# Optimization experiments

Measured on AMD Instinct MI355X. Metric: run time of the kernel, lower is better.

The kernel has to match this reference:

```python
import jax, jax.numpy as jnp
import numpy as np

N = 65536      # nodes
E = 32768      # edges
H = 256        # hidden_features
B = 64         # graphs
NPG = 1024     # nodes per graph
K = 24         # padded subgraph index width
ELEM = 24      # 2 * len(ORDERED_ELEMENT_LIST_WITH_HYDROGEN) (assumed 12 elements)
EMB = 200
STAT = 32
D = 2 * H + (2 * H + ELEM) + EMB + STAT  # 1280, dense hidden dim
OUT = 512
DEPTH = 3


def setup_inputs() -> dict:
    key = jax.random.key(0)
    ks = jax.random.split(key, 12)
    X = jax.random.normal(ks[0], (N, H), jnp.float32)
    edge_index = jax.random.randint(ks[1], (2, E), 0, N)
    batch_vec = jnp.arange(N) // NPG                  # node -> graph id (sorted)
    ptr = jnp.arange(B + 1) * NPG                     # graph node offsets
    subgraph_idx_left = jax.random.randint(ks[2], (E, K), -1, NPG)   # -1 = padding
    subgraph_idx_right = jax.random.randint(ks[3], (E, K), -1, NPG)
    edge_elem_comp = jax.random.uniform(ks[4], (E, ELEM), jnp.float32)
    edge_embedding = jax.random.normal(ks[5], (E, EMB), jnp.float32)
    static_edge_features = jax.random.normal(ks[6], (E, STAT), jnp.float32)
    s = 1.0 / np.sqrt(D)
    Wd = jax.random.normal(ks[7], (DEPTH, D, D), jnp.float32) * s
    bd = jax.random.normal(ks[8], (DEPTH, D), jnp.float32) * s
    Wo = jax.random.normal(ks[9], (D, OUT), jnp.float32) * s
    bo = jax.random.normal(ks[10], (OUT,), jnp.float32) * s
    return dict(X=X, edge_index=edge_index, batch_vec=batch_vec, ptr=ptr,
                subgraph_idx_left=subgraph_idx_left, subgraph_idx_right=subgraph_idx_right,
                edge_elem_comp=edge_elem_comp, edge_embedding=edge_embedding,
                static_edge_features=static_edge_features, Wd=Wd, bd=bd, Wo=Wo, bo=bo)


def _mean_pool(X, idx_abs, num_edges):
    # masked segment-mean of node rows into per-edge slots (global_mean_pool)
    e, k = idx_abs.shape
    seg = jnp.repeat(jnp.arange(e), k)                # edge id per flattened index
    flat = idx_abs.reshape(-1)
    mask = (flat != -1).astype(X.dtype)               # mask after ptr offset, as in source
    gathered = X[flat] * mask[:, None]                # negative idx wraps, matching torch
    sums = jax.ops.segment_sum(gathered, seg, num_segments=num_edges)
    counts = jax.ops.segment_sum(mask, seg, num_segments=num_edges)
    return jnp.where(counts[:, None] > 0, sums / jnp.maximum(counts, 1.0)[:, None], 0.0)


def reference(X, edge_index, batch_vec, ptr, subgraph_idx_left, subgraph_idx_right,
              edge_elem_comp, edge_embedding, static_edge_features, Wd, bd, Wo, bo):
    src, dst = edge_index[0], edge_index[1]
    node_pairs = jnp.concatenate([X[src], X[dst]], axis=1)            # [E, 2H]
    edge_batch_map = batch_vec[src]                                   # [E]
    off = ptr[edge_batch_map][:, None]                                # [E, 1]
    pooled_left = _mean_pool(X, subgraph_idx_left + off, E)           # [E, H]
    pooled_right = _mean_pool(X, subgraph_idx_right + off, E)         # [E, H]
    feats = jnp.concatenate([node_pairs, pooled_left, pooled_right, edge_elem_comp,
                             edge_embedding, static_edge_features], axis=1)  # [E, D]
    h = feats
    for i in range(Wd.shape[0]):
        h = jax.nn.elu(h @ Wd[i] + bd[i]) + h         # ELU + residual (dropout=0 eval)
    return h @ Wo + bo
```

## Files before the change

### kernel.cpp

```cpp
#include <hip/hip_runtime.h>
#include <math.h>

#define NN   65536
#define EE   32768
#define HH   256
#define KK   24
#define DDIM 1280
#define OUTD 512
#define KT   (DDIM / 32)
#define GCAP 1024

typedef _Float16 half8 __attribute__((ext_vector_type(8)));
typedef _Float16 half4 __attribute__((ext_vector_type(4)));
typedef float    f32x4 __attribute__((ext_vector_type(4)));

__device__ __forceinline__ float elu1(float x) { return x > 0.f ? x : expm1f(x); }

__device__ __forceinline__ void gl16(const void* g, void* l) {
    __builtin_amdgcn_global_load_lds(
        (const __attribute__((address_space(1))) void*)g,
        (__attribute__((address_space(3))) void*)l, 16, 0, 0);
}

__global__ __launch_bounds__(256) void prep_kernel(
    const float* __restrict__ Wd, const float* __restrict__ Wo,
    const float* __restrict__ X,
    _Float16* __restrict__ W16d, _Float16* __restrict__ W16o,
    _Float16* __restrict__ X16, int* __restrict__ cnt)
{
    const int b = blockIdx.x;
    const int lane = threadIdx.x & 63;
    if (b < 2400) {
        const int l = b / 800;
        const int s = (b % 800) * 4 + (threadIdx.x >> 6);
        const int nt = s & 7, nb = (s >> 3) % 10, kt = s / 80;
        const int kbase = kt * 32 + 8 * (lane >> 4);
        const int n     = nb * 128 + nt * 16 + (lane & 15);
        const float* W = Wd + (size_t)l * DDIM * DDIM;
        half8 v;
        #pragma unroll
        for (int j = 0; j < 8; ++j) v[j] = (_Float16)W[(size_t)(kbase + j) * DDIM + n];
        ((half8*)(W16d + (size_t)l * DDIM * DDIM))[(size_t)s * 64 + lane] = v;
    } else if (b < 2720) {
        const int s = (b - 2400) * 4 + (threadIdx.x >> 6);
        const int nt = s & 7, nb = (s >> 3) % 4, kt = s / 32;
        const int kbase = kt * 32 + 8 * (lane >> 4);
        const int n     = nb * 128 + nt * 16 + (lane & 15);
        half8 v;
        #pragma unroll
        for (int j = 0; j < 8; ++j) v[j] = (_Float16)Wo[(size_t)(kbase + j) * OUTD + n];
        ((half8*)W16o)[(size_t)s * 64 + lane] = v;
    } else if (b == 2720) {
        if (threadIdx.x < 64) cnt[threadIdx.x] = 0;
    } else {
        const int a = b - 2721;
        const int r  = a * 16 + (threadIdx.x >> 4);
        const int c0 = (threadIdx.x & 15) * 16;
        const float4* s4 = (const float4*)(X + (size_t)r * HH + c0);
        const float4 f0 = s4[0], f1 = s4[1], f2 = s4[2], f3 = s4[3];
        half8 o0, o1;
        o0[0]=(_Float16)f0.x; o0[1]=(_Float16)f0.y; o0[2]=(_Float16)f0.z; o0[3]=(_Float16)f0.w;
        o0[4]=(_Float16)f1.x; o0[5]=(_Float16)f1.y; o0[6]=(_Float16)f1.z; o0[7]=(_Float16)f1.w;
        o1[0]=(_Float16)f2.x; o1[1]=(_Float16)f2.y; o1[2]=(_Float16)f2.z; o1[3]=(_Float16)f2.w;
        o1[4]=(_Float16)f3.x; o1[5]=(_Float16)f3.y; o1[6]=(_Float16)f3.z; o1[7]=(_Float16)f3.w;
        *(half8*)(X16 + (size_t)r * HH + c0)     = o0;
        *(half8*)(X16 + (size_t)r * HH + c0 + 8) = o1;
    }
}

__global__ __launch_bounds__(256) void scatter_kernel(
    const int* __restrict__ src_idx, const int* __restrict__ batch_vec,
    int* __restrict__ perm, int* __restrict__ cnt, int nE)
{
    __shared__ int lc[64];
    __shared__ int lbase[64];
    const int tid = threadIdx.x;
    if (tid < 64) lc[tid] = 0;
    __syncthreads();
    const int e = blockIdx.x * 256 + tid;
    int g = -1, li = 0;
    if (e < nE) {
        g = batch_vec[src_idx[e]];
        li = atomicAdd(&lc[g], 1);
    }
    __syncthreads();
    if (tid < 64 && lc[tid] > 0) lbase[tid] = atomicAdd(&cnt[tid], lc[tid]);
    __syncthreads();
    if (e >= nE) return;
    const int idx = lbase[g] + li;
    if (idx < GCAP) perm[g * GCAP + idx] = e;
}

__global__ __launch_bounds__(256) void feats16_kernel(
    const _Float16* __restrict__ X16, const int* __restrict__ perm,
    const int* __restrict__ cnt,
    const int* __restrict__ src_idx, const int* __restrict__ dst_idx,
    const int* __restrict__ ptrv,
    const int* __restrict__ sl, const int* __restrict__ sr,
    const float* __restrict__ elem, const float* __restrict__ emb,
    const float* __restrict__ stat,
    _Float16* __restrict__ F16)
{
    const int b  = blockIdx.x;
    const int x  = b & 7;
    const int j  = b >> 3;
    const int g  = x + 8 * (j >> 8);
    const int jj = j & 255;
    const int slot = jj * 4 + (threadIdx.x >> 6);
    const int ng = min(cnt[g], GCAP);
    if (slot >= ng) return;
    const int e = perm[g * GCAP + slot];

    const int lane = threadIdx.x & 63;
    const int src  = src_idx[e];
    const int dst  = dst_idx[e];
    const int off  = ptrv[g];

    const half4* Xh = (const half4*)X16;

    const size_t hb = ((size_t)(e >> 7) * 40) * 4096
                    + (size_t)((e & 127) >> 4) * 512
                    + (size_t)((e & 15) + (((lane >> 1) & 3) << 4)) * 8 + (lane & 1) * 4;
    const size_t hkt = (size_t)(lane >> 3) * 4096;
#define STH(seg, hv)                                                          \
    *(half4*)(F16 + hb + ((size_t)(seg) * 8) * 4096 + hkt) = (hv);
#define STF(seg, v)                                                           \
    {                                                                         \
        half4 h_;                                                             \
        h_[0] = (_Float16)(v).x; h_[1] = (_Float16)(v).y;                     \
        h_[2] = (_Float16)(v).z; h_[3] = (_Float16)(v).w;                     \
        STH(seg, h_);                                                         \
    }

    STH(0, Xh[(size_t)src * 64 + lane]);
    STH(1, Xh[(size_t)dst * 64 + lane]);

    float4 sL = make_float4(0.f, 0.f, 0.f, 0.f);
    float4 sR = make_float4(0.f, 0.f, 0.f, 0.f);
    int cL = 0, cR = 0;
    #pragma unroll
    for (int k = 0; k < KK; ++k) {
        const int il  = sl[e * KK + k] + off;
        const int ir  = sr[e * KK + k] + off;
        const int okL = il >= 0;
        const int okR = ir >= 0;
        const float wL = okL ? 1.f : 0.f;
        const float wR = okR ? 1.f : 0.f;
        const half4 vl = Xh[(size_t)(okL ? il : 0) * 64 + lane];
        const half4 vr = Xh[(size_t)(okR ? ir : 0) * 64 + lane];
        sL.x += (float)vl[0] * wL; sL.y += (float)vl[1] * wL;
        sL.z += (float)vl[2] * wL; sL.w += (float)vl[3] * wL;
        sR.x += (float)vr[0] * wR; sR.y += (float)vr[1] * wR;
        sR.z += (float)vr[2] * wR; sR.w += (float)vr[3] * wR;
        cL += okL; cR += okR;
    }
    const float rL = cL > 0 ? 1.f / (float)cL : 0.f;
    const float rR = cR > 0 ? 1.f / (float)cR : 0.f;
    STF(2, make_float4(sL.x * rL, sL.y * rL, sL.z * rL, sL.w * rL));
    STF(3, make_float4(sR.x * rR, sR.y * rR, sR.z * rR, sR.w * rR));

    float4 tail;
    if (lane < 6)       tail = ((const float4*)(elem + (size_t)e * 24))[lane];
    else if (lane < 56) tail = ((const float4*)(emb  + (size_t)e * 200))[lane - 6];
    else                tail = ((const float4*)(stat + (size_t)e * 32))[lane - 56];
    STF(4, tail);
#undef STF
#undef STH
}

template<bool RESID, bool OUT32, bool H16>
__global__ __launch_bounds__(256) void mfma_gemm7(
    const _Float16* __restrict__ A16,
    const _Float16* __restrict__ W16, const float* __restrict__ bias,
    float* __restrict__ C32, _Float16* __restrict__ C16,
    int N, int nbN)
{
    __shared__ __align__(16) char sA[3][8192];
    __shared__ __align__(16) char sB[3][8192];

    const int t    = threadIdx.x;
    const int wid  = t >> 6;
    const int lane = t & 63;

    int m_t, n_t;
    if ((gridDim.y & 7) == 0) {
        const int flat = blockIdx.y * gridDim.x + blockIdx.x;
        m_t = (flat & 7) + 8 * (flat / (8 * gridDim.x));
        n_t = (flat >> 3) % gridDim.x;
    } else {
        m_t = blockIdx.y; n_t = blockIdx.x;
    }

    f32x4 acc[2][8];
    #pragma unroll
    for (int i = 0; i < 2; ++i)
        #pragma unroll
        for (int j = 0; j < 8; ++j) acc[i][j] = (f32x4){0.f, 0.f, 0.f, 0.f};

    _Float16 resv[4][2][2][4];

    const char* Abase = (const char*)A16 + (size_t)m_t * KT * 8192;
    const char* Bbase = (const char*)W16;

#define STAGE(d, ktv)                                                           \
    {                                                                           \
        const char* Ak = Abase + (size_t)(ktv) * 8192 + wid * 1024 + lane * 16; \
        const char* Bk = Bbase + ((size_t)(ktv) * nbN + n_t) * 8192             \
                         + wid * 1024 + lane * 16;                              \
        gl16(Ak,        sA[d] + wid * 1024);                                    \
        gl16(Ak + 4096, sA[d] + (4 + wid) * 1024);                              \
        gl16(Bk,        sB[d] + wid * 1024);                                    \
        gl16(Bk + 4096, sB[d] + (4 + wid) * 1024);                              \
    }

    STAGE(0, 0);
    STAGE(1, 1);
    STAGE(2, 2);

    int cur = 0;
    for (int kt = 0; kt < KT; ++kt) {
        if (kt + 2 < KT)      asm volatile("s_waitcnt vmcnt(8)" ::: "memory");
        else if (kt + 1 < KT) asm volatile("s_waitcnt vmcnt(4)" ::: "memory");
        else                  asm volatile("s_waitcnt vmcnt(0)" ::: "memory");
        __builtin_amdgcn_sched_barrier(0);
        __builtin_amdgcn_s_barrier();
        __builtin_amdgcn_sched_barrier(0);

        const half8* pa = (const half8*)sA[cur];
        const half8* pb = (const half8*)sB[cur];
        const half8 af0 = pa[(2 * wid)     * 64 + lane];
        const half8 af1 = pa[(2 * wid + 1) * 64 + lane];
        half8 bf[8];
        #pragma unroll
        for (int j = 0; j < 8; ++j) bf[j] = pb[j * 64 + lane];

        if (RESID) {
            #pragma unroll
            for (int q = 0; q < 4; ++q) {
                if (kt == n_t * 4 + q) {
                    #pragma unroll
                    for (int i = 0; i < 2; ++i)
                        #pragma unroll
                        for (int jj = 0; jj < 2; ++jj)
                            #pragma unroll
                            for (int r = 0; r < 4; ++r) {
                                const int chunk = ((lane >> 4) * 4 + r)
                                                + 16 * (jj * 2 + ((lane >> 3) & 1));
                                resv[q][i][jj][r] = *(const _Float16*)
                                    (sA[cur] + (wid * 2 + i) * 1024
                                             + chunk * 16 + (lane & 7) * 2);
                            }
                }
            }
        }

        asm volatile("s_waitcnt lgkmcnt(0)" ::: "memory");
        __builtin_amdgcn_sched_barrier(0);
        __builtin_amdgcn_s_barrier();
        __builtin_amdgcn_sched_barrier(0);

        if (kt + 3 < KT) STAGE(cur, kt + 3);
        __builtin_amdgcn_sched_barrier(0);

        __builtin_amdgcn_s_setprio(1);
        #pragma unroll
        for (int j = 0; j < 8; ++j) {
            acc[0][j] = __builtin_amdgcn_mfma_f32_16x16x32_f16(af0, bf[j], acc[0][j], 0, 0, 0);
            acc[1][j] = __builtin_amdgcn_mfma_f32_16x16x32_f16(af1, bf[j], acc[1][j], 0, 0, 0);
        }
        __builtin_amdgcn_s_setprio(0);

        cur = (cur == 2) ? 0 : cur + 1;
    }
#undef STAGE

    if (H16) {
        char* Cb = (char*)C16 + ((size_t)m_t * 40 + n_t * 4) * 8192;
        #pragma unroll
        for (int q = 0; q < 4; ++q) {
            #pragma unroll
            for (int i = 0; i < 2; ++i)
                #pragma unroll
                for (int jj = 0; jj < 2; ++jj) {
                    const int j = 2 * q + jj;
                    const int col = n_t * 128 + j * 16 + (lane & 15);
                    const float bv = bias[col];
                    #pragma unroll
                    for (int r = 0; r < 4; ++r) {
                        float v = acc[i][j][r] + bv;
                        v = elu1(v) + (float)resv[q][i][jj][r];
                        const int chunk = ((lane >> 4) * 4 + r)
                                        + 16 * (jj * 2 + ((lane >> 3) & 1));
                        *(_Float16*)(sA[0] + (wid * 2 + i) * 1024
                                           + chunk * 16 + (lane & 7) * 2)
                            = (_Float16)v;
                    }
                }
            __syncthreads();
            *(uint4*)(Cb + (size_t)q * 8192 + t * 32) =
                *(const uint4*)(sA[0] + t * 32);
            *(uint4*)(Cb + (size_t)q * 8192 + t * 32 + 16) =
                *(const uint4*)(sA[0] + t * 32 + 16);
            __syncthreads();
        }
    } else {
        const int m0 = m_t * 128;
        #pragma unroll
        for (int i = 0; i < 2; ++i) {
            #pragma unroll
            for (int j = 0; j < 8; ++j) {
                const int col = n_t * 128 + j * 16 + (lane & 15);
                const float bv = bias[col];
                #pragma unroll
                for (int r = 0; r < 4; ++r) {
                    const int row = m0 + wid * 32 + i * 16 + (lane >> 4) * 4 + r;
                    float v = acc[i][j][r] + bv;
                    if (OUT32) C32[(size_t)row * N + col] = v;
                }
            }
        }
    }
}

extern "C" void kernel_launch(void* const* d_in, const int* in_sizes, int n_in,
                              void* d_out, int out_size, void* d_ws, size_t ws_size,
                              hipStream_t stream) {
    const float* X          = (const float*)d_in[0];
    const int*   edge_index = (const int*)d_in[1];
    const int*   batch_vec  = (const int*)d_in[2];
    const int*   ptrv       = (const int*)d_in[3];
    const int*   sl         = (const int*)d_in[4];
    const int*   sr         = (const int*)d_in[5];
    const float* elem       = (const float*)d_in[6];
    const float* emb        = (const float*)d_in[7];
    const float* stat       = (const float*)d_in[8];
    const float* Wd         = (const float*)d_in[9];
    const float* bd         = (const float*)d_in[10];
    const float* Wo         = (const float*)d_in[11];
    const float* bo         = (const float*)d_in[12];
    float* out = (float*)d_out;

    _Float16* W16d = (_Float16*)d_ws;
    _Float16* W16o = W16d + (size_t)3 * DDIM * DDIM;
    _Float16* X16  = W16o + (size_t)DDIM * OUTD;
    int* perm = (int*)(X16 + (size_t)NN * HH);
    int* cnt  = perm + (size_t)64 * GCAP;
    char* hbase = (char*)(cnt + 64);
    hbase = (char*)(((size_t)hbase + 255) & ~(size_t)255);
    const size_t rem = ws_size - (size_t)(hbase - (char*)d_ws);

    int CH = EE;
    while (CH > 2048 && (size_t)CH * DDIM * 4 > rem) CH >>= 1;
    _Float16* f16a = (_Float16*)hbase;
    _Float16* f16b = f16a + (size_t)CH * DDIM;

    prep_kernel<<<2721 + NN / 16, 256, 0, stream>>>(Wd, Wo, X, W16d, W16o, X16, cnt);

    for (int e0 = 0; e0 < EE; e0 += CH) {
        scatter_kernel<<<CH / 256, 256, 0, stream>>>(
            edge_index + e0, batch_vec, perm, cnt, CH);

        feats16_kernel<<<64 * (GCAP / 4), 256, 0, stream>>>(
            X16, perm, cnt, edge_index + e0, edge_index + EE + e0, ptrv,
            sl + (size_t)e0 * KK, sr + (size_t)e0 * KK,
            elem + (size_t)e0 * 24, emb + (size_t)e0 * 200,
            stat + (size_t)e0 * 32, f16a);

        dim3 gd(10, CH / 128);
        mfma_gemm7<true, false, true><<<gd, 256, 0, stream>>>(
            f16a, W16d + 0 * (size_t)DDIM * DDIM, bd + 0 * DDIM,
            nullptr, f16b, DDIM, 10);
        mfma_gemm7<true, false, true><<<gd, 256, 0, stream>>>(
            f16b, W16d + 1 * (size_t)DDIM * DDIM, bd + 1 * DDIM,
            nullptr, f16a, DDIM, 10);
        mfma_gemm7<true, false, true><<<gd, 256, 0, stream>>>(
            f16a, W16d + 2 * (size_t)DDIM * DDIM, bd + 2 * DDIM,
            nullptr, f16b, DDIM, 10);

        dim3 go(4, CH / 128);
        mfma_gemm7<false, true, false><<<go, 256, 0, stream>>>(
            f16b, W16o, bo, out + (size_t)e0 * OUTD, nullptr, OUTD, 4);
    }
}
```

Before: 704.8 us.

## Compact edges by graph, stage feature rows in LDS, unpermute on output

Adds prefix and compact kernels that build a dense graph-sorted edge ordering. The feature kernel processes 16 sorted edges per block, stages their rows in shared memory, and writes coalesced tiles into the GEMM's tiled A layout. Rows are no longer scattered by edge id. The final GEMM scatters output rows back to original edge order through the permutation. The aim is better locality for the node gathers and coalesced feature writes, at the cost of two extra small launches and scattered output stores. The sperm identity initialisation in prep appears to be overwritten by compact.

```diff
diff --git a/kernel.cpp b/kernel.cpp
--- a/kernel.cpp
+++ b/kernel.cpp
@@ -9,6 +9,7 @@
 #define OUTD 512
 #define KT   (DDIM / 32)
 #define GCAP 1024
+#define RSTRIDE 1296
 
 typedef _Float16 half8 __attribute__((ext_vector_type(8)));
 typedef _Float16 half4 __attribute__((ext_vector_type(4)));
@@ -26,7 +27,8 @@
     const float* __restrict__ Wd, const float* __restrict__ Wo,
     const float* __restrict__ X,
     _Float16* __restrict__ W16d, _Float16* __restrict__ W16o,
-    _Float16* __restrict__ X16, int* __restrict__ cnt)
+    _Float16* __restrict__ X16, int* __restrict__ cnt,
+    int* __restrict__ sperm)
 {
     const int b = blockIdx.x;
     const int lane = threadIdx.x & 63;
@@ -52,7 +54,7 @@
         ((half8*)W16o)[(size_t)s * 64 + lane] = v;
     } else if (b == 2720) {
         if (threadIdx.x < 64) cnt[threadIdx.x] = 0;
-    } else {
+    } else if (b < 6817) {
         const int a = b - 2721;
         const int r  = a * 16 + (threadIdx.x >> 4);
         const int c0 = (threadIdx.x & 15) * 16;
@@ -65,6 +67,10 @@
         o1[4]=(_Float16)f3.x; o1[5]=(_Float16)f3.y; o1[6]=(_Float16)f3.z; o1[7]=(_Float16)f3.w;
         *(half8*)(X16 + (size_t)r * HH + c0)     = o0;
         *(half8*)(X16 + (size_t)r * HH + c0 + 8) = o1;
+    } else {
+        const int i0 = (b - 6817) * 1024 + threadIdx.x * 4;
+        if (i0 < EE)
+            *(int4*)(sperm + i0) = make_int4(i0, i0 + 1, i0 + 2, i0 + 3);
     }
 }
 
@@ -91,81 +97,116 @@
     if (idx < GCAP) perm[g * GCAP + idx] = e;
 }
 
-__global__ __launch_bounds__(256) void feats16_kernel(
-    const _Float16* __restrict__ X16, const int* __restrict__ perm,
-    const int* __restrict__ cnt,
+__global__ __launch_bounds__(64) void prefix_kernel(
+    const int* __restrict__ cnt, int* __restrict__ prefixv)
+{
+    if (threadIdx.x == 0) {
+        int acc = 0;
+        for (int g = 0; g < 64; ++g) {
+            prefixv[g] = acc;
+            acc += min(cnt[g], GCAP);
+        }
+        prefixv[64] = acc;
+    }
+}
+
+__global__ __launch_bounds__(256) void compact_kernel(
+    const int* __restrict__ perm, const int* __restrict__ cnt,
+    const int* __restrict__ prefixv, int* __restrict__ sperm)
+{
+    const int id = blockIdx.x * 256 + threadIdx.x;
+    const int g = id >> 10, idx = id & (GCAP - 1);
+    if (idx < min(cnt[g], GCAP))
+        sperm[prefixv[g] + idx] = perm[id];
+}
+
+__global__ __launch_bounds__(256) void feats16t_kernel(
+    const _Float16* __restrict__ X16, const int* __restrict__ sperm,
     const int* __restrict__ src_idx, const int* __restrict__ dst_idx,
-    const int* __restrict__ ptrv,
+    const int* __restrict__ batch_vec, const int* __restrict__ ptrv,
     const int* __restrict__ sl, const int* __restrict__ sr,
     const float* __restrict__ elem, const float* __restrict__ emb,
     const float* __restrict__ stat,
     _Float16* __restrict__ F16)
 {
-    const int b  = blockIdx.x;
-    const int x  = b & 7;
-    const int j  = b >> 3;
-    const int g  = x + 8 * (j >> 8);
-    const int jj = j & 255;
-    const int slot = jj * 4 + (threadIdx.x >> 6);
-    const int ng = min(cnt[g], GCAP);
-    if (slot >= ng) return;
-    const int e = perm[g * GCAP + slot];
-
+    __shared__ _Float16 rows[16][RSTRIDE];
+
+    const int p  = blockIdx.x;
+    int lb = p;
+    if ((gridDim.x & 7) == 0) {
+        const int chunkb = gridDim.x >> 3;
+        lb = (p & 7) * chunkb + (p >> 3);
+    }
+    const int wv   = threadIdx.x >> 6;
     const int lane = threadIdx.x & 63;
-    const int src  = src_idx[e];
-    const int dst  = dst_idx[e];
-    const int off  = ptrv[g];
+    const int s0   = lb * 16;
 
     const half4* Xh = (const half4*)X16;
 
-    const size_t hb = ((size_t)(e >> 7) * 40) * 4096
-                    + (size_t)((e & 127) >> 4) * 512
-                    + (size_t)((e & 15) + (((lane >> 1) & 3) << 4)) * 8 + (lane & 1) * 4;
-    const size_t hkt = (size_t)(lane >> 3) * 4096;
-#define STH(seg, hv)                                                          \
-    *(half4*)(F16 + hb + ((size_t)(seg) * 8) * 4096 + hkt) = (hv);
-#define STF(seg, v)                                                           \
-    {                                                                         \
-        half4 h_;                                                             \
-        h_[0] = (_Float16)(v).x; h_[1] = (_Float16)(v).y;                     \
-        h_[2] = (_Float16)(v).z; h_[3] = (_Float16)(v).w;                     \
-        STH(seg, h_);                                                         \
-    }
-
-    STH(0, Xh[(size_t)src * 64 + lane]);
-    STH(1, Xh[(size_t)dst * 64 + lane]);
-
-    float4 sL = make_float4(0.f, 0.f, 0.f, 0.f);
-    float4 sR = make_float4(0.f, 0.f, 0.f, 0.f);
-    int cL = 0, cR = 0;
     #pragma unroll
-    for (int k = 0; k < KK; ++k) {
-        const int il  = sl[e * KK + k] + off;
-        const int ir  = sr[e * KK + k] + off;
-        const int okL = il >= 0;
-        const int okR = ir >= 0;
-        const float wL = okL ? 1.f : 0.f;
-        const float wR = okR ? 1.f : 0.f;
-        const half4 vl = Xh[(size_t)(okL ? il : 0) * 64 + lane];
-        const half4 vr = Xh[(size_t)(okR ? ir : 0) * 64 + lane];
-        sL.x += (float)vl[0] * wL; sL.y += (float)vl[1] * wL;
-        sL.z += (float)vl[2] * wL; sL.w += (float)vl[3] * wL;
-        sR.x += (float)vr[0] * wR; sR.y += (float)vr[1] * wR;
-        sR.z += (float)vr[2] * wR; sR.w += (float)vr[3] * wR;
-        cL += okL; cR += okR;
-    }
-    const float rL = cL > 0 ? 1.f / (float)cL : 0.f;
-    const float rR = cR > 0 ? 1.f / (float)cR : 0.f;
-    STF(2, make_float4(sL.x * rL, sL.y * rL, sL.z * rL, sL.w * rL));
-    STF(3, make_float4(sR.x * rR, sR.y * rR, sR.z * rR, sR.w * rR));
-
-    float4 tail;
-    if (lane < 6)       tail = ((const float4*)(elem + (size_t)e * 24))[lane];
-    else if (lane < 56) tail = ((const float4*)(emb  + (size_t)e * 200))[lane - 6];
-    else                tail = ((const float4*)(stat + (size_t)e * 32))[lane - 56];
-    STF(4, tail);
-#undef STF
-#undef STH
+    for (int it = 0; it < 4; ++it) {
+        const int r = wv * 4 + it;
+        const int e = sperm[s0 + r];
+        const int src = src_idx[e];
+        const int dst = dst_idx[e];
+        const int off = ptrv[batch_vec[src]];
+        _Float16* row = &rows[r][0];
+
+        *(half4*)(row + 0 * 256 + lane * 4) = Xh[(size_t)src * 64 + lane];
+        *(half4*)(row + 1 * 256 + lane * 4) = Xh[(size_t)dst * 64 + lane];
+
+        float4 sL = make_float4(0.f, 0.f, 0.f, 0.f);
+        float4 sR = make_float4(0.f, 0.f, 0.f, 0.f);
+        int cL = 0, cR = 0;
+        #pragma unroll
+        for (int k = 0; k < KK; ++k) {
+            const int il  = sl[e * KK + k] + off;
+            const int ir  = sr[e * KK + k] + off;
+            const int okL = il >= 0;
+            const int okR = ir >= 0;
+            const float wL = okL ? 1.f : 0.f;
+            const float wR = okR ? 1.f : 0.f;
+            const half4 vl = Xh[(size_t)(okL ? il : 0) * 64 + lane];
+            const half4 vr = Xh[(size_t)(okR ? ir : 0) * 64 + lane];
+            sL.x += (float)vl[0] * wL; sL.y += (float)vl[1] * wL;
+            sL.z += (float)vl[2] * wL; sL.w += (float)vl[3] * wL;
+            sR.x += (float)vr[0] * wR; sR.y += (float)vr[1] * wR;
+            sR.z += (float)vr[2] * wR; sR.w += (float)vr[3] * wR;
+            cL += okL; cR += okR;
+        }
+        const float rL = cL > 0 ? 1.f / (float)cL : 0.f;
+        const float rR = cR > 0 ? 1.f / (float)cR : 0.f;
+        half4 h2, h3;
+        h2[0]=(_Float16)(sL.x*rL); h2[1]=(_Float16)(sL.y*rL);
+        h2[2]=(_Float16)(sL.z*rL); h2[3]=(_Float16)(sL.w*rL);
+        h3[0]=(_Float16)(sR.x*rR); h3[1]=(_Float16)(sR.y*rR);
+        h3[2]=(_Float16)(sR.z*rR); h3[3]=(_Float16)(sR.w*rR);
+        *(half4*)(row + 2 * 256 + lane * 4) = h2;
+        *(half4*)(row + 3 * 256 + lane * 4) = h3;
+
+        float4 tail;
+        if (lane < 6)       tail = ((const float4*)(elem + (size_t)e * 24))[lane];
+        else if (lane < 56) tail = ((const float4*)(emb  + (size_t)e * 200))[lane - 6];
+        else                tail = ((const float4*)(stat + (size_t)e * 32))[lane - 56];
+        half4 h4;
+        h4[0]=(_Float16)tail.x; h4[1]=(_Float16)tail.y;
+        h4[2]=(_Float16)tail.z; h4[3]=(_Float16)tail.w;
+        *(half4*)(row + 4 * 256 + lane * 4) = h4;
+    }
+
+    __syncthreads();
+
+    const int t = threadIdx.x;
+    const size_t mt  = (size_t)(s0 >> 7) * KT;
+    const int    sr8 = (s0 >> 4) & 7;
+    #pragma unroll
+    for (int i = 0; i < 10; ++i) {
+        const int gc = i * 256 + t;
+        const int kt = gc >> 6;
+        const int c  = gc & 63;
+        const uint4 v = *(const uint4*)&rows[c & 15][kt * 32 + (c >> 4) * 8];
+        *(uint4*)(F16 + ((mt + kt) * 4096 + (size_t)sr8 * 512 + (size_t)c * 8)) = v;
+    }
 }
 
 template<bool RESID, bool OUT32, bool H16>
@@ -173,6 +214,7 @@
     const _Float16* __restrict__ A16,
     const _Float16* __restrict__ W16, const float* __restrict__ bias,
     float* __restrict__ C32, _Float16* __restrict__ C16,
+    const int* __restrict__ operm,
     int N, int nbN)
 {
     __shared__ __align__(16) char sA[3][8192];
@@ -315,7 +357,10 @@
                 for (int r = 0; r < 4; ++r) {
                     const int row = m0 + wid * 32 + i * 16 + (lane >> 4) * 4 + r;
                     float v = acc[i][j][r] + bv;
-                    if (OUT32) C32[(size_t)row * N + col] = v;
+                    if (OUT32) {
+                        const int erow = operm[row];
+                        C32[(size_t)erow * N + col] = v;
+                    }
                 }
             }
         }
@@ -343,9 +388,11 @@
     _Float16* W16d = (_Float16*)d_ws;
     _Float16* W16o = W16d + (size_t)3 * DDIM * DDIM;
     _Float16* X16  = W16o + (size_t)DDIM * OUTD;
-    int* perm = (int*)(X16 + (size_t)NN * HH);
-    int* cnt  = perm + (size_t)64 * GCAP;
-    char* hbase = (char*)(cnt + 64);
+    int* perm    = (int*)(X16 + (size_t)NN * HH);
+    int* cnt     = perm + (size_t)64 * GCAP;
+    int* prefixv = cnt + 64;
+    int* sperm   = prefixv + 80;
+    char* hbase  = (char*)(sperm + EE);
     hbase = (char*)(((size_t)hbase + 255) & ~(size_t)255);
     const size_t rem = ws_size - (size_t)(hbase - (char*)d_ws);
 
@@ -354,14 +401,18 @@
     _Float16* f16a = (_Float16*)hbase;
     _Float16* f16b = f16a + (size_t)CH * DDIM;
 
-    prep_kernel<<<2721 + NN / 16, 256, 0, stream>>>(Wd, Wo, X, W16d, W16o, X16, cnt);
+    prep_kernel<<<6849, 256, 0, stream>>>(Wd, Wo, X, W16d, W16o, X16, cnt, sperm);
 
     for (int e0 = 0; e0 < EE; e0 += CH) {
         scatter_kernel<<<CH / 256, 256, 0, stream>>>(
             edge_index + e0, batch_vec, perm, cnt, CH);
-
-        feats16_kernel<<<64 * (GCAP / 4), 256, 0, stream>>>(
-            X16, perm, cnt, edge_index + e0, edge_index + EE + e0, ptrv,
+        prefix_kernel<<<1, 64, 0, stream>>>(cnt, prefixv);
+        compact_kernel<<<64 * GCAP / 256, 256, 0, stream>>>(
+            perm, cnt, prefixv, sperm);
+
+        feats16t_kernel<<<CH / 16, 256, 0, stream>>>(
+            X16, sperm, edge_index + e0, edge_index + EE + e0,
+            batch_vec, ptrv,
             sl + (size_t)e0 * KK, sr + (size_t)e0 * KK,
             elem + (size_t)e0 * 24, emb + (size_t)e0 * 200,
             stat + (size_t)e0 * 32, f16a);
@@ -369,16 +420,16 @@
         dim3 gd(10, CH / 128);
         mfma_gemm7<true, false, true><<<gd, 256, 0, stream>>>(
             f16a, W16d + 0 * (size_t)DDIM * DDIM, bd + 0 * DDIM,
-            nullptr, f16b, DDIM, 10);
+            nullptr, f16b, nullptr, DDIM, 10);
         mfma_gemm7<true, false, true><<<gd, 256, 0, stream>>>(
             f16b, W16d + 1 * (size_t)DDIM * DDIM, bd + 1 * DDIM,
-            nullptr, f16a, DDIM, 10);
+            nullptr, f16a, nullptr, DDIM, 10);
         mfma_gemm7<true, false, true><<<gd, 256, 0, stream>>>(
             f16a, W16d + 2 * (size_t)DDIM * DDIM, bd + 2 * DDIM,
-            nullptr, f16b, DDIM, 10);
+            nullptr, f16b, nullptr, DDIM, 10);
 
         dim3 go(4, CH / 128);
         mfma_gemm7<false, true, false><<<go, 256, 0, stream>>>(
-            f16b, W16o, bo, out + (size_t)e0 * OUTD, nullptr, OUTD, 4);
-    }
-}
+            f16b, W16o, bo, out + (size_t)e0 * OUTD, nullptr, sperm, OUTD, 4);
+    }
+}
```

After: 645.3 us. 8.4% less time.
